# Kernel tuning notes

Measured on AMD Instinct MI355X. Metric: run time of the kernel, lower is better.

Reference implementation:

```python
import jax, jax.numpy as jnp
import numpy as np

NUM_GENES = 4000
NUM_PATCHES = 64
EMBED_DIM = 192
NUM_CELLS = 4096


def setup_inputs() -> dict:
    key = jax.random.key(0)
    k1, k2, k3, k4 = jax.random.split(key, 4)
    x = jax.random.normal(k1, (NUM_CELLS, NUM_GENES), dtype=jnp.float32)
    # binary gene->pathway membership mask [num_genes, num_patches]
    mask = jax.random.randint(k2, (NUM_GENES, NUM_PATCHES), 0, 2).astype(jnp.float32)
    W = jax.random.normal(k3, (NUM_GENES, NUM_PATCHES * EMBED_DIM), dtype=jnp.float32) * 0.02
    b = jax.random.normal(k4, (NUM_PATCHES * EMBED_DIM,), dtype=jnp.float32) * 0.02
    return {"x": x, "mask": mask, "W": W, "b": b}


def reference(x, mask, W, b):
    # Expand mask as in __init__: np.repeat(mask, embed_dim, axis=1)
    # -> column j belongs to pathway j // embed_dim.
    mask_rep = jnp.repeat(mask, EMBED_DIM, axis=1)  # [genes, patches*embed]
    # CustomizedLinear: dense matmul with statically masked weight.
    out = x @ (W * mask_rep) + b  # [cells, patches*embed]
    # rearrange 'h (w c) -> h c w' with c = num_patches
    out = out.reshape(NUM_CELLS, EMBED_DIM, NUM_PATCHES).transpose(0, 2, 1)
    # norm_layer=None -> Identity
    return out  # [cells, num_patches, embed_dim]
```

## Files before the change

### kernel.cpp

```cpp
#include <hip/hip_runtime.h>
#include <hip/hip_bf16.h>

#define M_CELLS 4096
#define N_GENES 4000
#define KP      4032
#define NKT     63
#define N_OUT   12288
#define EMB     192
#define NPATCH  64

#define BM 256
#define BN 256
#define BK 64
#define BTILE (BN * BK)

typedef __attribute__((ext_vector_type(8))) short bf16x8_t;
typedef __attribute__((ext_vector_type(8))) unsigned short u16x8_t;
typedef __attribute__((ext_vector_type(4))) float f32x4_t;

__device__ __forceinline__ unsigned short f2bf(float f) {
  __hip_bfloat16 h = __float2bfloat16(f);
  return *reinterpret_cast<unsigned short*>(&h);
}

__device__ __forceinline__ void gll16(const unsigned short* g, unsigned short* l) {
  __builtin_amdgcn_global_load_lds(
      (const __attribute__((address_space(1))) void*)g,
      (__attribute__((address_space(3))) void*)l, 16, 0, 0);
}

__global__ __launch_bounds__(256) void prep_fused(const float* __restrict__ x,
                                                  const float* __restrict__ mask,
                                                  const float* __restrict__ W,
                                                  unsigned short* __restrict__ A,
                                                  unsigned short* __restrict__ Bt) {
  __shared__ unsigned short sT[256 * 72];
  __shared__ float smask[256];
  const int t = threadIdx.x;
  if (blockIdx.x < 1024) {
    const int NG = M_CELLS * (KP / 8);
    for (int g = blockIdx.x * 256 + t; g < NG; g += 1024 * 256) {
      int row = g / (KP / 8);
      int kc  = g - row * (KP / 8);
      int k   = kc * 8;
      u16x8_t v;
      if (k < N_GENES) {
        float4 f0 = *reinterpret_cast<const float4*>(x + (size_t)row * N_GENES + k);
        float4 f1 = *reinterpret_cast<const float4*>(x + (size_t)row * N_GENES + k + 4);
        v[0] = f2bf(f0.x); v[1] = f2bf(f0.y); v[2] = f2bf(f0.z); v[3] = f2bf(f0.w);
        v[4] = f2bf(f1.x); v[5] = f2bf(f1.y); v[6] = f2bf(f1.z); v[7] = f2bf(f1.w);
      } else {
        v = (u16x8_t)0;
      }
      *reinterpret_cast<u16x8_t*>(A + (size_t)row * KP + k) = v;
    }
  } else {
    const int idx = blockIdx.x - 1024;
    const int jb  = idx % 48;
    const int kt  = idx / 48;
    const int q   = t & 63;
    const int o   = t >> 6;
    const int pwbase = (jb * 256) / EMB;
    {
      const int kg_l = t & 63;
      const int pwi  = t >> 6;
      const int kg   = kt * 64 + kg_l;
      const int pw   = pwbase + pwi;
      float mv = 0.f;
      if (kg < N_GENES && pw < NPATCH) mv = mask[kg * NPATCH + pw];
      smask[kg_l * 4 + pwi] = mv;
    }
    __syncthreads();
    const int jbase = jb * 256 + q * 4;
    int pwi_[4];
#pragma unroll
    for (int dj = 0; dj < 4; ++dj) pwi_[dj] = (jbase + dj) / EMB - pwbase;

    u16x8_t hreg[4][2];
#pragma unroll
    for (int hb = 0; hb < 2; ++hb) {
#pragma unroll
      for (int kk8 = 0; kk8 < 8; ++kk8) {
        const int kk = hb * 8 + kk8;
        const int kg = kt * 64 + o * 16 + kk;
        float4 f;
        if (kg < N_GENES) f = *reinterpret_cast<const float4*>(W + (size_t)kg * N_OUT + jbase);
        else              f = make_float4(0.f, 0.f, 0.f, 0.f);
        const float fv[4] = {f.x, f.y, f.z, f.w};
#pragma unroll
        for (int dj = 0; dj < 4; ++dj) {
          float m = smask[(o * 16 + kk) * 4 + pwi_[dj]];
          hreg[dj][hb][kk8] = f2bf(fv[dj] * m);
        }
      }
    }
#pragma unroll
    for (int dj = 0; dj < 4; ++dj) {
      const int jl = q * 4 + dj;
#pragma unroll
      for (int hb = 0; hb < 2; ++hb) {
        const int s = (o * 2 + hb) ^ ((jl >> 2) & 7) ^ ((jl >> 5) & 7);
        *reinterpret_cast<u16x8_t*>(&sT[jl * 72 + s * 8]) = hreg[dj][hb];
      }
    }
    __syncthreads();
#pragma unroll
    for (int it = 0; it < 8; ++it) {
      const int f  = it * 256 + t;
      const int p  = f >> 5, u = f & 31;
      const int el = u >> 3;
      const int r  = el * 64 + p;
      const int s  = (u & 7) ^ ((r >> 2) & 7) ^ ((r >> 5) & 7);
      u16x8_t v = *reinterpret_cast<const u16x8_t*>(&sT[r * 72 + s * 8]);
      const int jp0 = p * EMB + jb * 4;
      const int nt  = jp0 >> 8, c = jp0 & 255;
      *reinterpret_cast<u16x8_t*>(&Bt[(size_t)(nt * NKT + kt) * BTILE + (size_t)c * 64 + u * 8]) = v;
    }
  }
}

#define ABASE(buf, ks) (((buf) * 2 + (ks)) * 8192)
#define BBASE(buf, ks) (32768 + ((buf) * 2 + (ks)) * 8192)

__global__ __launch_bounds__(512, 2) void gemm_bf16(const unsigned short* __restrict__ A,
                                                    const unsigned short* __restrict__ Bt,
                                                    const float* __restrict__ bias,
                                                    float* __restrict__ out) {
  __shared__ unsigned short lds[65536];

  const int tid  = threadIdx.x;
  const int lane = tid & 63;
  const int wid  = tid >> 6;
  const int wm   = wid >> 2;
  const int wn   = wid & 3;
  const int lr   = lane & 15;
  const int hi   = lane >> 4;
  const int swz  = (lr >> 1) & 3;

  const int bid = blockIdx.x;
  const int xcd = bid & 7;
  const int l   = bid >> 3;
  const int mt  = l & 15;
  const int nt  = xcd * 6 + (l >> 4);
  const int m0  = mt * BM;
  const int n0  = nt * BN;

  const int aoff = (wm * 128 + lr) * 32 + ((hi ^ swz) << 3);
  const int boff = (wn * 64 + lr) * 32 + ((hi ^ swz) << 3);

  const int srow = tid >> 2;
  const int ssl  = ((tid & 3) ^ ((tid >> 3) & 3)) << 3;
  const unsigned short* aS0 = A + (size_t)(m0 + srow) * KP + ssl;
  const unsigned short* aS1 = aS0 + (size_t)128 * KP;
  const unsigned short* bS0 = Bt + (size_t)nt * NKT * BTILE + (size_t)srow * 64 + ssl;
  const unsigned short* bS1 = bS0 + 8192;

#define STAGE_A(kt, kh, buf) { \
    gll16(aS0 + (kt) * 64 + (kh) * 32, &lds[ABASE(buf, kh) + tid * 8]); \
    gll16(aS1 + (kt) * 64 + (kh) * 32, &lds[ABASE(buf, kh) + 4096 + tid * 8]); }
#define STAGE_B(kt, kh, buf) { \
    gll16(bS0 + (size_t)(kt) * BTILE + (kh) * 32, &lds[BBASE(buf, kh) + tid * 8]); \
    gll16(bS1 + (size_t)(kt) * BTILE + (kh) * 32, &lds[BBASE(buf, kh) + 4096 + tid * 8]); }

#define RD_PA(buf, ks) { \
    afA[0] = *reinterpret_cast<const bf16x8_t*>(&lds[ABASE(buf, ks) + aoff]); \
    _Pragma("unroll") for (int n_ = 0; n_ < 4; ++n_) \
      bfr[n_] = *reinterpret_cast<const bf16x8_t*>(&lds[BBASE(buf, ks) + boff + n_ * 512]); \
    _Pragma("unroll") for (int m_ = 1; m_ < 4; ++m_) \
      afA[m_] = *reinterpret_cast<const bf16x8_t*>(&lds[ABASE(buf, ks) + aoff + m_ * 512]); }
#define RD_PB(buf, ks) \
    _Pragma("unroll") for (int m_ = 0; m_ < 4; ++m_) \
      afB[m_] = *reinterpret_cast<const bf16x8_t*>(&lds[ABASE(buf, ks) + aoff + (4 + m_) * 512]);

#define MM16A() \
    _Pragma("unroll") for (int m_ = 0; m_ < 4; ++m_) \
    _Pragma("unroll") for (int n_ = 0; n_ < 4; ++n_) \
      acc[m_][n_] = __builtin_amdgcn_mfma_f32_16x16x32_bf16(afA[m_], bfr[n_], acc[m_][n_], 0, 0, 0);
#define MM16B() \
    _Pragma("unroll") for (int m_ = 0; m_ < 4; ++m_) \
    _Pragma("unroll") for (int n_ = 0; n_ < 4; ++n_) \
      acc[4 + m_][n_] = __builtin_amdgcn_mfma_f32_16x16x32_bf16(afB[m_], bfr[n_], acc[4 + m_][n_], 0, 0, 0);

#define VMBAR(N) \
    asm volatile("s_waitcnt vmcnt(" #N ")" ::: "memory"); \
    __builtin_amdgcn_s_barrier(); \
    asm volatile("" ::: "memory")

  f32x4_t acc[8][4] = {};
  bf16x8_t afA[4], afB[4], bfr[4];

  STAGE_A(0, 0, 0); STAGE_B(0, 0, 0);
  STAGE_A(0, 1, 0); STAGE_B(0, 1, 0);
  STAGE_A(1, 0, 1); STAGE_B(1, 0, 1);
  VMBAR(8);

  for (int i = 0; i < 31; ++i) {
    const int tb = 2 * i + 1, tc = 2 * i + 2;
    const int td = (tb + 2 <= 62) ? tb + 2 : 62;

    STAGE_A(tb, 1, 1); STAGE_B(tb, 1, 1);
    RD_PA(0, 0); MM16A();
    RD_PB(0, 0); MM16B();
    VMBAR(8);
    STAGE_A(tc, 0, 0); STAGE_B(tc, 0, 0);
    RD_PA(0, 1); MM16A();
    RD_PB(0, 1); MM16B();
    VMBAR(8);
    STAGE_A(tc, 1, 0); STAGE_B(tc, 1, 0);
    RD_PA(1, 0); MM16A();
    RD_PB(1, 0); MM16B();
    VMBAR(8);
    STAGE_A(td, 0, 1); STAGE_B(td, 0, 1);
    RD_PA(1, 1); MM16A();
    RD_PB(1, 1); MM16B();
    VMBAR(8);
  }

  RD_PA(0, 0); MM16A();
  RD_PB(0, 0); MM16B();
  VMBAR(4);
  RD_PA(0, 1); MM16A();
  RD_PB(0, 1); MM16B();
  asm volatile("s_waitcnt vmcnt(0)" ::: "memory");
  __builtin_amdgcn_s_barrier();

#pragma unroll
  for (int n = 0; n < 4; ++n) {
    int jc = n0 + wn * 64 + n * 16 + lr;
    float bv = bias[(jc % EMB) * NPATCH + (jc / EMB)];
#pragma unroll
    for (int m = 0; m < 8; ++m) {
      int row = m0 + wm * 128 + m * 16 + hi * 4;
      float* o = out + (size_t)row * N_OUT + jc;
#pragma unroll
      for (int r = 0; r < 4; ++r)
        o[(size_t)r * N_OUT] = acc[m][n][r] + bv;
    }
  }
}

__global__ __launch_bounds__(256) void fallback_gemm(const float* __restrict__ x,
                                                     const float* __restrict__ mask,
                                                     const float* __restrict__ W,
                                                     const float* __restrict__ b,
                                                     float* __restrict__ out) {
  __shared__ float sX[64 * 33];
  __shared__ float sB2[32 * 65];
  const int t  = threadIdx.x;
  const int c0 = blockIdx.x * 64;
  const int j0 = blockIdx.y * 64;
  const int tr = t >> 4, tc = t & 15;
  float acc[4][4] = {};
  for (int k0 = 0; k0 < N_GENES; k0 += 32) {
    __syncthreads();
#pragma unroll
    for (int i = 0; i < 8; ++i) {
      int f = i * 256 + t;
      int row = f >> 5, kk = f & 31;
      sX[row * 33 + kk] = x[(size_t)(c0 + row) * N_GENES + k0 + kk];
    }
#pragma unroll
    for (int i = 0; i < 8; ++i) {
      int f = i * 256 + t;
      int kk = f >> 6, cl = f & 63;
      int jp = j0 + cl;
      int jorig = (jp % EMB) * NPATCH + jp / EMB;
      sB2[kk * 65 + cl] = W[(size_t)(k0 + kk) * N_OUT + jorig] * mask[(k0 + kk) * NPATCH + jorig / EMB];
    }
    __syncthreads();
#pragma unroll
    for (int kk = 0; kk < 32; ++kk) {
      float a[4], bb[4];
#pragma unroll
      for (int r = 0; r < 4; ++r) a[r] = sX[(tr * 4 + r) * 33 + kk];
#pragma unroll
      for (int c = 0; c < 4; ++c) bb[c] = sB2[kk * 65 + tc * 4 + c];
#pragma unroll
      for (int r = 0; r < 4; ++r)
#pragma unroll
        for (int c = 0; c < 4; ++c) acc[r][c] += a[r] * bb[c];
    }
  }
#pragma unroll
  for (int r = 0; r < 4; ++r)
#pragma unroll
    for (int c = 0; c < 4; ++c) {
      int jp = j0 + tc * 4 + c;
      int jorig = (jp % EMB) * NPATCH + jp / EMB;
      out[(size_t)(c0 + tr * 4 + r) * N_OUT + jp] = acc[r][c] + b[jorig];
    }
}

extern "C" void kernel_launch(void* const* d_in, const int* in_sizes, int n_in,
                              void* d_out, int out_size, void* d_ws, size_t ws_size,
                              hipStream_t stream) {
  const float* x    = (const float*)d_in[0];
  const float* mask = (const float*)d_in[1];
  const float* W    = (const float*)d_in[2];
  const float* b    = (const float*)d_in[3];
  float* out = (float*)d_out;

  const size_t needA = (size_t)M_CELLS * KP * sizeof(unsigned short);
  const size_t needB = (size_t)N_OUT * KP * sizeof(unsigned short);

  if (ws_size >= needA + needB) {
    unsigned short* Abf = (unsigned short*)d_ws;
    unsigned short* Bt  = (unsigned short*)((char*)d_ws + needA);
    prep_fused<<<4048, 256, 0, stream>>>(x, mask, W, Abf, Bt);
    gemm_bf16<<<768, 512, 0, stream>>>(Abf, Bt, b, out);
  } else {
    fallback_gemm<<<dim3(64, 192), 256, 0, stream>>>(x, mask, W, b, out);
  }
}
```

Baseline: 428.4 us.

## Switch GEMM to 256x128 tiles with triple-buffered half-K LDS pipeline

Retiles the bf16 GEMM from 256x256 tiles with 8 waves to 256x128 tiles with 4 waves, each wave computing 64x128. The B pre-layout in the prep kernel changes to match the 128-wide N tiles. The main loop becomes a 3-slot ring buffer over 32-wide K half-steps instead of a 2x2 double buffer. Each block then stages less operand data and holds less LDS, aiming for better overlap and more blocks per CU, at the cost of less reuse of the A operand per B load and twice as many blocks.

```diff
diff --git a/kernel.cpp b/kernel.cpp
--- a/kernel.cpp
+++ b/kernel.cpp
@@ -8,11 +8,6 @@
 #define N_OUT   12288
 #define EMB     192
 #define NPATCH  64
-
-#define BM 256
-#define BN 256
-#define BK 64
-#define BTILE (BN * BK)
 
 typedef __attribute__((ext_vector_type(8))) short bf16x8_t;
 typedef __attribute__((ext_vector_type(8))) unsigned short u16x8_t;
@@ -113,26 +108,23 @@
       const int s  = (u & 7) ^ ((r >> 2) & 7) ^ ((r >> 5) & 7);
       u16x8_t v = *reinterpret_cast<const u16x8_t*>(&sT[r * 72 + s * 8]);
       const int jp0 = p * EMB + jb * 4;
-      const int nt  = jp0 >> 8, c = jp0 & 255;
-      *reinterpret_cast<u16x8_t*>(&Bt[(size_t)(nt * NKT + kt) * BTILE + (size_t)c * 64 + u * 8]) = v;
-    }
-  }
-}
-
-#define ABASE(buf, ks) (((buf) * 2 + (ks)) * 8192)
-#define BBASE(buf, ks) (32768 + ((buf) * 2 + (ks)) * 8192)
-
-__global__ __launch_bounds__(512, 2) void gemm_bf16(const unsigned short* __restrict__ A,
+      const int nt2 = jp0 >> 7, c = jp0 & 127;
+      *reinterpret_cast<u16x8_t*>(&Bt[(size_t)(nt2 * NKT + kt) * 8192 + (size_t)c * 64 + u * 8]) = v;
+    }
+  }
+}
+
+#define SLOT_E 12288
+
+__global__ __launch_bounds__(256, 2) void gemm_bf16(const unsigned short* __restrict__ A,
                                                     const unsigned short* __restrict__ Bt,
                                                     const float* __restrict__ bias,
                                                     float* __restrict__ out) {
-  __shared__ unsigned short lds[65536];
+  __shared__ unsigned short lds[3 * SLOT_E];
 
   const int tid  = threadIdx.x;
   const int lane = tid & 63;
-  const int wid  = tid >> 6;
-  const int wm   = wid >> 2;
-  const int wn   = wid & 3;
+  const int w    = tid >> 6;
   const int lr   = lane & 15;
   const int hi   = lane >> 4;
   const int swz  = (lr >> 1) & 3;
@@ -141,96 +133,78 @@
   const int xcd = bid & 7;
   const int l   = bid >> 3;
   const int mt  = l & 15;
-  const int nt  = xcd * 6 + (l >> 4);
-  const int m0  = mt * BM;
-  const int n0  = nt * BN;
-
-  const int aoff = (wm * 128 + lr) * 32 + ((hi ^ swz) << 3);
-  const int boff = (wn * 64 + lr) * 32 + ((hi ^ swz) << 3);
-
-  const int srow = tid >> 2;
-  const int ssl  = ((tid & 3) ^ ((tid >> 3) & 3)) << 3;
-  const unsigned short* aS0 = A + (size_t)(m0 + srow) * KP + ssl;
-  const unsigned short* aS1 = aS0 + (size_t)128 * KP;
-  const unsigned short* bS0 = Bt + (size_t)nt * NKT * BTILE + (size_t)srow * 64 + ssl;
-  const unsigned short* bS1 = bS0 + 8192;
-
-#define STAGE_A(kt, kh, buf) { \
-    gll16(aS0 + (kt) * 64 + (kh) * 32, &lds[ABASE(buf, kh) + tid * 8]); \
-    gll16(aS1 + (kt) * 64 + (kh) * 32, &lds[ABASE(buf, kh) + 4096 + tid * 8]); }
-#define STAGE_B(kt, kh, buf) { \
-    gll16(bS0 + (size_t)(kt) * BTILE + (kh) * 32, &lds[BBASE(buf, kh) + tid * 8]); \
-    gll16(bS1 + (size_t)(kt) * BTILE + (kh) * 32, &lds[BBASE(buf, kh) + 4096 + tid * 8]); }
-
-#define RD_PA(buf, ks) { \
-    afA[0] = *reinterpret_cast<const bf16x8_t*>(&lds[ABASE(buf, ks) + aoff]); \
-    _Pragma("unroll") for (int n_ = 0; n_ < 4; ++n_) \
-      bfr[n_] = *reinterpret_cast<const bf16x8_t*>(&lds[BBASE(buf, ks) + boff + n_ * 512]); \
+  const int nt2 = xcd * 12 + (l >> 4);
+  const int m0  = mt * 256;
+  const int n0  = nt2 * 128;
+
+  const int aoff = (w * 64 + lr) * 32 + ((hi ^ swz) << 3);
+  const int boff = lr * 32 + ((hi ^ swz) << 3);
+
+  const unsigned short* aS[4];
+#pragma unroll
+  for (int i = 0; i < 4; ++i) {
+    const int ch = i * 256 + tid;
+    const int ar = ch >> 2, as_ = ch & 3;
+    aS[i] = A + (size_t)(m0 + ar) * KP + ((as_ ^ ((ar >> 1) & 3)) << 3);
+  }
+  const unsigned short* bS[2];
+#pragma unroll
+  for (int i = 0; i < 2; ++i) {
+    const int ch = i * 256 + tid;
+    const int br = ch >> 2, bs_ = ch & 3;
+    bS[i] = Bt + (size_t)nt2 * NKT * 8192 + br * 64 + ((bs_ ^ ((br >> 1) & 3)) << 3);
+  }
+
+#define STAGE(st, slot) { \
+    const int kt_ = (st) >> 1, h_ = ((st) & 1) * 32; \
+    _Pragma("unroll") for (int i_ = 0; i_ < 4; ++i_) \
+      gll16(aS[i_] + kt_ * 64 + h_, &lds[(slot) * SLOT_E + (i_ * 256 + tid) * 8]); \
+    _Pragma("unroll") for (int i_ = 0; i_ < 2; ++i_) \
+      gll16(bS[i_] + (size_t)kt_ * 8192 + h_, &lds[(slot) * SLOT_E + 8192 + (i_ * 256 + tid) * 8]); }
+
+#define RD(slot) { \
+    const unsigned short* sb_ = &lds[(slot) * SLOT_E]; \
+    af[0] = *reinterpret_cast<const bf16x8_t*>(sb_ + aoff); \
+    _Pragma("unroll") for (int n_ = 0; n_ < 8; ++n_) \
+      bf[n_] = *reinterpret_cast<const bf16x8_t*>(sb_ + 8192 + boff + n_ * 512); \
     _Pragma("unroll") for (int m_ = 1; m_ < 4; ++m_) \
-      afA[m_] = *reinterpret_cast<const bf16x8_t*>(&lds[ABASE(buf, ks) + aoff + m_ * 512]); }
-#define RD_PB(buf, ks) \
+      af[m_] = *reinterpret_cast<const bf16x8_t*>(sb_ + aoff + m_ * 512); }
+
+#define MM32() \
     _Pragma("unroll") for (int m_ = 0; m_ < 4; ++m_) \
-      afB[m_] = *reinterpret_cast<const bf16x8_t*>(&lds[ABASE(buf, ks) + aoff + (4 + m_) * 512]);
-
-#define MM16A() \
-    _Pragma("unroll") for (int m_ = 0; m_ < 4; ++m_) \
-    _Pragma("unroll") for (int n_ = 0; n_ < 4; ++n_) \
-      acc[m_][n_] = __builtin_amdgcn_mfma_f32_16x16x32_bf16(afA[m_], bfr[n_], acc[m_][n_], 0, 0, 0);
-#define MM16B() \
-    _Pragma("unroll") for (int m_ = 0; m_ < 4; ++m_) \
-    _Pragma("unroll") for (int n_ = 0; n_ < 4; ++n_) \
-      acc[4 + m_][n_] = __builtin_amdgcn_mfma_f32_16x16x32_bf16(afB[m_], bfr[n_], acc[4 + m_][n_], 0, 0, 0);
+    _Pragma("unroll") for (int n_ = 0; n_ < 8; ++n_) \
+      acc[m_][n_] = __builtin_amdgcn_mfma_f32_16x16x32_bf16(af[m_], bf[n_], acc[m_][n_], 0, 0, 0);
 
 #define VMBAR(N) \
     asm volatile("s_waitcnt vmcnt(" #N ")" ::: "memory"); \
     __builtin_amdgcn_s_barrier(); \
     asm volatile("" ::: "memory")
 
-  f32x4_t acc[8][4] = {};
-  bf16x8_t afA[4], afB[4], bfr[4];
-
-  STAGE_A(0, 0, 0); STAGE_B(0, 0, 0);
-  STAGE_A(0, 1, 0); STAGE_B(0, 1, 0);
-  STAGE_A(1, 0, 1); STAGE_B(1, 0, 1);
-  VMBAR(8);
-
-  for (int i = 0; i < 31; ++i) {
-    const int tb = 2 * i + 1, tc = 2 * i + 2;
-    const int td = (tb + 2 <= 62) ? tb + 2 : 62;
-
-    STAGE_A(tb, 1, 1); STAGE_B(tb, 1, 1);
-    RD_PA(0, 0); MM16A();
-    RD_PB(0, 0); MM16B();
-    VMBAR(8);
-    STAGE_A(tc, 0, 0); STAGE_B(tc, 0, 0);
-    RD_PA(0, 1); MM16A();
-    RD_PB(0, 1); MM16B();
-    VMBAR(8);
-    STAGE_A(tc, 1, 0); STAGE_B(tc, 1, 0);
-    RD_PA(1, 0); MM16A();
-    RD_PB(1, 0); MM16B();
-    VMBAR(8);
-    STAGE_A(td, 0, 1); STAGE_B(td, 0, 1);
-    RD_PA(1, 1); MM16A();
-    RD_PB(1, 1); MM16B();
-    VMBAR(8);
-  }
-
-  RD_PA(0, 0); MM16A();
-  RD_PB(0, 0); MM16B();
-  VMBAR(4);
-  RD_PA(0, 1); MM16A();
-  RD_PB(0, 1); MM16B();
+  f32x4_t acc[4][8] = {};
+  bf16x8_t af[4], bf[8];
+
+  STAGE(0, 0);
+  STAGE(1, 1);
+  VMBAR(6);
+
+  for (int i = 0; i < 41; ++i) {
+    const int s = 3 * i;
+    STAGE(s + 2, 2); RD(0); MM32(); VMBAR(6);
+    STAGE(s + 3, 0); RD(1); MM32(); VMBAR(6);
+    STAGE(s + 4, 1); RD(2); MM32(); VMBAR(6);
+  }
+  STAGE(125, 2); RD(0); MM32(); VMBAR(6);
+  STAGE(125, 0); RD(1); MM32(); VMBAR(6);
+  STAGE(125, 1); RD(2); MM32();
   asm volatile("s_waitcnt vmcnt(0)" ::: "memory");
-  __builtin_amdgcn_s_barrier();
-
-#pragma unroll
-  for (int n = 0; n < 4; ++n) {
-    int jc = n0 + wn * 64 + n * 16 + lr;
-    float bv = bias[(jc % EMB) * NPATCH + (jc / EMB)];
-#pragma unroll
-    for (int m = 0; m < 8; ++m) {
-      int row = m0 + wm * 128 + m * 16 + hi * 4;
+
+#pragma unroll
+  for (int n = 0; n < 8; ++n) {
+    const int jc = n0 + n * 16 + lr;
+    const float bv = bias[(jc % EMB) * NPATCH + (jc / EMB)];
+#pragma unroll
+    for (int m = 0; m < 4; ++m) {
+      const int row = m0 + w * 64 + m * 16 + hi * 4;
       float* o = out + (size_t)row * N_OUT + jc;
 #pragma unroll
       for (int r = 0; r < 4; ++r)
@@ -307,7 +281,7 @@
     unsigned short* Abf = (unsigned short*)d_ws;
     unsigned short* Bt  = (unsigned short*)((char*)d_ws + needA);
     prep_fused<<<4048, 256, 0, stream>>>(x, mask, W, Abf, Bt);
-    gemm_bf16<<<768, 512, 0, stream>>>(Abf, Bt, b, out);
+    gemm_bf16<<<1536, 256, 0, stream>>>(Abf, Bt, b, out);
   } else {
     fallback_gemm<<<dim3(64, 192), 256, 0, stream>>>(x, mask, W, b, out);
   }
```

Result: slower. 487.8 us (+13.9%).
